# Kernel optimization log

Hardware: AMD Instinct MI355X
Metric: run time of the kernel (lower is better)

## Reference

```python
import jax, jax.numpy as jnp
import numpy as np

DIM = 1024


def setup_inputs() -> dict:
    key = jax.random.key(0)
    k1, k2, k3, k4 = jax.random.split(key, 4)
    B, T, S, D = 32, 512, 1024, DIM
    inp = {
        "input": jax.random.normal(k1, (B, T, D), dtype=jnp.float32),
        "context": jax.random.normal(k2, (B, S, D), dtype=jnp.float32),
        # linear_in: nn.Linear(dim, dim, bias=False) -> weight [D, D]
        "W_in": jax.random.normal(k3, (D, D), dtype=jnp.float32) / np.sqrt(D),
        # linear_out: nn.Linear(2*dim, dim, bias=False for 'general') -> weight [D, 2D]
        "W_out": jax.random.normal(k4, (D, 2 * D), dtype=jnp.float32) / np.sqrt(2 * D),
    }
    return inp


def reference(input, context, W_in, W_out):
    # score: general -> h_t = linear_in(input); align = bmm(h_t, context^T)
    h_t = jnp.einsum("btd,ed->bte", input, W_in)              # [B,T,D]
    align = jnp.einsum("btd,bsd->bts", h_t, context)          # [B,T,S]
    align_vectors = jax.nn.softmax(align, axis=-1)            # [B,T,S]
    c = jnp.einsum("bts,bsd->btd", align_vectors, context)    # [B,T,D]
    concat_c = jnp.concatenate([c, input], axis=2)            # [B,T,2D]
    attn_h = jnp.tanh(jnp.einsum("btf,df->btd", concat_c, W_out))  # [B,T,D]
    # multi-step path: transpose to (tgt_len, batch, ...)
    attn_h = jnp.transpose(attn_h, (1, 0, 2))
    concat_c = jnp.transpose(concat_c, (1, 0, 2))
    align_vectors = jnp.transpose(align_vectors, (1, 0, 2))
    return attn_h, align_vectors, concat_c
```

## Files before the change

### kernel.cpp

```cpp
#include <hip/hip_runtime.h>
#include <cmath>

#define BATCH 32
#define TLEN  512
#define SLEN  1024
#define DIM   1024

#define BM 128
#define BN 128
#define BK 32

typedef _Float16 h8 __attribute__((ext_vector_type(8)));
typedef _Float16 h4 __attribute__((ext_vector_type(4)));
typedef _Float16 h2 __attribute__((ext_vector_type(2)));
typedef float f4 __attribute__((ext_vector_type(4)));


__device__ __forceinline__ void gload16(const _Float16* g, _Float16* l) {
  __builtin_amdgcn_global_load_lds(
      (const __attribute__((address_space(1))) unsigned int*)g,
      (__attribute__((address_space(3))) unsigned int*)l, 16, 0, 0);
}

template <int EPI>
__global__ __launch_bounds__(256) void gemm16(
    const _Float16* __restrict__ A, const _Float16* __restrict__ Bm,
    float* __restrict__ C, _Float16* __restrict__ C16, int K,
    long lda, long ldb, long ldc, long ldc16,
    long strideA, long strideB, long strideC, long strideC16) {
  __shared__ _Float16 As[BM * BK];
  __shared__ _Float16 Bs[BN * BK];

  const int bz = blockIdx.z;
  A += (long)bz * strideA;
  Bm += (long)bz * strideB;

  const int m0 = blockIdx.y * BM;
  const int n0 = blockIdx.x * BN;
  const int tid = threadIdx.x;
  const int lane = tid & 63;
  const int wave = tid >> 6;
  const int q = lane >> 4;
  const int r = lane & 15;
  const int wm = (wave >> 1) * 64;
  const int wn = (wave & 1) * 64;

  f4 acc[4][4];
#pragma unroll
  for (int i = 0; i < 4; ++i)
#pragma unroll
    for (int j = 0; j < 4; ++j) acc[i][j] = (f4){0.f, 0.f, 0.f, 0.f};

  const int c0 = wave * 64 + lane;
  const int c1 = 256 + wave * 64 + lane;
  const _Float16* gA0 = A + (long)(m0 + (c0 >> 2)) * lda + (c0 & 3) * 8;
  const _Float16* gA1 = A + (long)(m0 + (c1 >> 2)) * lda + (c1 & 3) * 8;
  const _Float16* gB0 = Bm + (long)(n0 + (c0 >> 2)) * ldb + (c0 & 3) * 8;
  const _Float16* gB1 = Bm + (long)(n0 + (c1 >> 2)) * ldb + (c1 & 3) * 8;
  _Float16* lA0 = As + wave * 512;
  _Float16* lA1 = As + 2048 + wave * 512;
  _Float16* lB0 = Bs + wave * 512;
  _Float16* lB1 = Bs + 2048 + wave * 512;

  for (int k0 = 0; k0 < K; k0 += BK) {
    gload16(gA0 + k0, lA0);
    gload16(gA1 + k0, lA1);
    gload16(gB0 + k0, lB0);
    gload16(gB1 + k0, lB1);
    __syncthreads();

    h8 av[4], bv[4];
#pragma unroll
    for (int mt = 0; mt < 4; ++mt)
      av[mt] = *(const h8*)&As[(wm + mt * 16 + r) * BK + q * 8];
#pragma unroll
    for (int nt = 0; nt < 4; ++nt)
      bv[nt] = *(const h8*)&Bs[(wn + nt * 16 + r) * BK + q * 8];
#pragma unroll
    for (int mt = 0; mt < 4; ++mt)
#pragma unroll
      for (int nt = 0; nt < 4; ++nt)
        acc[mt][nt] = __builtin_amdgcn_mfma_f32_16x16x32_f16(
            av[mt], bv[nt], acc[mt][nt], 0, 0, 0);
    __syncthreads();
  }

#pragma unroll
  for (int mt = 0; mt < 4; ++mt) {
#pragma unroll
    for (int nt = 0; nt < 4; ++nt) {
#pragma unroll
      for (int i = 0; i < 4; ++i) {
        float x = acc[mt][nt][i];
        const long row = m0 + wm + mt * 16 + q * 4 + i;
        const long col = n0 + wn + nt * 16 + r;
        if constexpr (EPI == 1) x = tanhf(x);
        if constexpr (EPI == 0 || EPI == 1 || EPI == 3)
          C[(long)bz * strideC + row * ldc + col] = x;
        if constexpr (EPI == 2 || EPI == 3)
          C16[(long)bz * strideC16 + row * ldc16 + col] = (_Float16)x;
      }
    }
  }
}

__global__ __launch_bounds__(256) void cvt_f32_f16(
    const float* __restrict__ in, _Float16* __restrict__ out, long n) {
  long i = ((long)blockIdx.x * 256 + threadIdx.x) * 4;
  const long stride = (long)gridDim.x * 1024;
  for (; i < n; i += stride) {
    float4 v = *(const float4*)(in + i);
    h4 hv = {(_Float16)v.x, (_Float16)v.y, (_Float16)v.z, (_Float16)v.w};
    *(h4*)(out + i) = hv;
  }
}

#define CTPAD 66
__global__ __launch_bounds__(256) void ctx_cvt(
    const float* __restrict__ ctx, _Float16* __restrict__ c16,
    _Float16* __restrict__ c16t) {
  __shared__ _Float16 tile[64 * CTPAD];
  const int b = blockIdx.z;
  const int s0 = blockIdx.y * 64;
  const int d0 = blockIdx.x * 64;
  const int tr = threadIdx.x >> 4;
  const int tc = (threadIdx.x & 15) * 4;
#pragma unroll
  for (int i = 0; i < 4; ++i) {
    const int s = i * 16 + tr;
    float4 v = *(const float4*)(ctx + ((long)b * SLEN + s0 + s) * DIM + d0 + tc);
    h4 hv = {(_Float16)v.x, (_Float16)v.y, (_Float16)v.z, (_Float16)v.w};
    *(h4*)(c16 + ((long)b * SLEN + s0 + s) * DIM + d0 + tc) = hv;
    tile[s * CTPAD + tc] = hv.x;
    tile[s * CTPAD + tc + 1] = hv.y;
    tile[s * CTPAD + tc + 2] = hv.z;
    tile[s * CTPAD + tc + 3] = hv.w;
  }
  __syncthreads();
#pragma unroll
  for (int i = 0; i < 4; ++i) {
    const int d = i * 16 + tr;
    h4 hv = {tile[tc * CTPAD + d], tile[(tc + 1) * CTPAD + d],
             tile[(tc + 2) * CTPAD + d], tile[(tc + 3) * CTPAD + d]};
    *(h4*)(c16t + ((long)b * DIM + d0 + d) * SLEN + s0 + tc) = hv;
  }
}


#define AS_LD 40
#define B2_LD 134

template <bool B_IS_NT, bool TANH>
__global__ __launch_bounds__(256) void gemm_f16(
    const float* __restrict__ A, const float* __restrict__ Bm,
    float* __restrict__ C, int M, int N, int K, long lda, long ldb, long ldc,
    long strideA, long strideB, long strideC) {
  __shared__ _Float16 As[BM * AS_LD];
  __shared__ _Float16 Bs[BM * AS_LD];

  const int bz = blockIdx.z;
  A += (long)bz * strideA;
  Bm += (long)bz * strideB;
  C += (long)bz * strideC;

  const int m0 = blockIdx.y * BM;
  const int n0 = blockIdx.x * BN;
  const int tid = threadIdx.x;
  const int lane = tid & 63;
  const int wave = tid >> 6;
  const int wm = (wave >> 1) * 64;
  const int wn = (wave & 1) * 64;
  const int q = lane >> 4;
  const int r = lane & 15;

  f4 acc[4][4];
#pragma unroll
  for (int i = 0; i < 4; ++i)
#pragma unroll
    for (int j = 0; j < 4; ++j) acc[i][j] = (f4){0.f, 0.f, 0.f, 0.f};

  const int srow = tid >> 3;
  const int skq = (tid & 7) * 4;
  const int nrow = tid >> 5;
  const int nnq = (tid & 31) * 4;

  for (int k0 = 0; k0 < K; k0 += BK) {
#pragma unroll
    for (int it = 0; it < 4; ++it) {
      const int row = it * 32 + srow;
      f4 v = *(const f4*)(A + (long)(m0 + row) * lda + k0 + skq);
      h4 hv = {(_Float16)v.x, (_Float16)v.y, (_Float16)v.z, (_Float16)v.w};
      *(h4*)&As[row * AS_LD + skq] = hv;
    }
    if (B_IS_NT) {
#pragma unroll
      for (int it = 0; it < 4; ++it) {
        const int row = it * 32 + srow;
        f4 v = *(const f4*)(Bm + (long)(n0 + row) * ldb + k0 + skq);
        h4 hv = {(_Float16)v.x, (_Float16)v.y, (_Float16)v.z, (_Float16)v.w};
        *(h4*)&Bs[row * AS_LD + skq] = hv;
      }
    } else {
#pragma unroll
      for (int it = 0; it < 4; ++it) {
        const int krow = it * 8 + nrow;
        f4 v = *(const f4*)(Bm + (long)(k0 + krow) * ldb + n0 + nnq);
        _Float16* p = &Bs[krow * B2_LD + nnq];
        *(h2*)p = (h2){(_Float16)v.x, (_Float16)v.y};
        *(h2*)(p + 2) = (h2){(_Float16)v.z, (_Float16)v.w};
      }
    }
    __syncthreads();

    h8 av[4], bv[4];
#pragma unroll
    for (int mt = 0; mt < 4; ++mt)
      av[mt] = *(const h8*)&As[(wm + mt * 16 + r) * AS_LD + q * 8];
    if (B_IS_NT) {
#pragma unroll
      for (int nt = 0; nt < 4; ++nt)
        bv[nt] = *(const h8*)&Bs[(wn + nt * 16 + r) * AS_LD + q * 8];
    } else {
#pragma unroll
      for (int nt = 0; nt < 4; ++nt) {
        h8 t;
#pragma unroll
        for (int j = 0; j < 8; ++j)
          t[j] = Bs[(q * 8 + j) * B2_LD + wn + nt * 16 + r];
        bv[nt] = t;
      }
    }
#pragma unroll
    for (int mt = 0; mt < 4; ++mt)
#pragma unroll
      for (int nt = 0; nt < 4; ++nt)
        acc[mt][nt] = __builtin_amdgcn_mfma_f32_16x16x32_f16(
            av[mt], bv[nt], acc[mt][nt], 0, 0, 0);
    __syncthreads();
  }

#pragma unroll
  for (int mt = 0; mt < 4; ++mt) {
#pragma unroll
    for (int nt = 0; nt < 4; ++nt) {
#pragma unroll
      for (int i = 0; i < 4; ++i) {
        float x = acc[mt][nt][i];
        if (TANH) x = tanhf(x);
        C[(long)(m0 + wm + mt * 16 + q * 4 + i) * ldc + n0 + wn + nt * 16 + r] = x;
      }
    }
  }
}


__global__ __launch_bounds__(256) void softmax_kernel(
    float* __restrict__ data, _Float16* __restrict__ p16) {
  float* row = data + (long)blockIdx.x * SLEN;
  const int tid = threadIdx.x;
  float4 v = ((float4*)row)[tid];
  float m = fmaxf(fmaxf(v.x, v.y), fmaxf(v.z, v.w));
#pragma unroll
  for (int off = 32; off > 0; off >>= 1) m = fmaxf(m, __shfl_xor(m, off));
  __shared__ float redm[4];
  __shared__ float reds[4];
  if ((tid & 63) == 0) redm[tid >> 6] = m;
  __syncthreads();
  m = fmaxf(fmaxf(redm[0], redm[1]), fmaxf(redm[2], redm[3]));
  v.x = expf(v.x - m);
  v.y = expf(v.y - m);
  v.z = expf(v.z - m);
  v.w = expf(v.w - m);
  float s = v.x + v.y + v.z + v.w;
#pragma unroll
  for (int off = 32; off > 0; off >>= 1) s += __shfl_xor(s, off);
  if ((tid & 63) == 0) reds[tid >> 6] = s;
  __syncthreads();
  s = reds[0] + reds[1] + reds[2] + reds[3];
  const float inv = 1.0f / s;
  v.x *= inv;
  v.y *= inv;
  v.z *= inv;
  v.w *= inv;
  ((float4*)row)[tid] = v;
  if (p16) {
    h4 hv = {(_Float16)v.x, (_Float16)v.y, (_Float16)v.z, (_Float16)v.w};
    *(h4*)(p16 + (long)blockIdx.x * SLEN + tid * 4) = hv;
  }
}

__global__ __launch_bounds__(256) void concat_copy_kernel(
    const float* __restrict__ in, float* __restrict__ concat,
    _Float16* __restrict__ c16) {
  const int bt = blockIdx.x;
  const int b = bt >> 9;
  const int t = bt & 511;
  const float4 v = ((const float4*)(in + (long)bt * DIM))[threadIdx.x];
  const long off = ((long)t * BATCH + b) * (2 * DIM) + DIM;
  ((float4*)(concat + off))[threadIdx.x] = v;
  if (c16) {
    h4 hv = {(_Float16)v.x, (_Float16)v.y, (_Float16)v.z, (_Float16)v.w};
    *(h4*)(c16 + off + threadIdx.x * 4) = hv;
  }
}


extern "C" void kernel_launch(void* const* d_in, const int* in_sizes, int n_in,
                              void* d_out, int out_size, void* d_ws,
                              size_t ws_size, hipStream_t stream) {
  const float* input = (const float*)d_in[0];
  const float* context = (const float*)d_in[1];
  const float* W_in = (const float*)d_in[2];
  const float* W_out = (const float*)d_in[3];

  float* out = (float*)d_out;
  float* attn_h = out;
  float* align = out + (long)TLEN * BATCH * DIM;
  float* concat = align + (long)TLEN * BATCH * SLEN;

  const long BT = (long)BATCH * TLEN;
  const long ND = (long)BATCH * TLEN * DIM;

  const size_t WS_NEED = (size_t)3 * 67108864 + 4194304;

  if (d_ws != nullptr && ws_size >= WS_NEED) {
    _Float16* ctx16 = (_Float16*)d_ws;
    _Float16* ctx16t = ctx16 + (long)BATCH * SLEN * DIM;
    _Float16* cat16 = ctx16t + (long)BATCH * SLEN * DIM;
    _Float16* wout16 = cat16 + (long)TLEN * BATCH * 2 * DIM;
    _Float16* in16 = (_Float16*)align;
    _Float16* win16 = in16 + ND;
    _Float16* ht16 = (_Float16*)attn_h;
    _Float16* p16 = ht16 + ND;

    cvt_f32_f16<<<2048, 256, 0, stream>>>(input, in16, ND);
    cvt_f32_f16<<<1024, 256, 0, stream>>>(W_in, win16, (long)DIM * DIM);
    cvt_f32_f16<<<2048, 256, 0, stream>>>(W_out, wout16, (long)DIM * 2 * DIM);
    ctx_cvt<<<dim3(16, 16, BATCH), 256, 0, stream>>>(context, ctx16, ctx16t);

    gemm16<2><<<dim3(DIM / BN, BT / BM, 1), 256, 0, stream>>>(
        in16, win16, nullptr, ht16, DIM,
         DIM,  DIM,  0,  DIM, 0, 0, 0, 0);

    gemm16<0><<<dim3(SLEN / BN, TLEN / BM, BATCH), 256, 0, stream>>>(
        ht16, ctx16, align, nullptr, DIM,
         DIM,  DIM,  (long)BATCH * SLEN,  0,
         (long)TLEN * DIM,  (long)SLEN * DIM,  SLEN, 0);

    softmax_kernel<<<(int)BT, 256, 0, stream>>>(align, p16);

    gemm16<3><<<dim3(DIM / BN, TLEN / BM, BATCH), 256, 0, stream>>>(
        p16, ctx16t, concat, cat16, SLEN,
         (long)BATCH * SLEN,  SLEN,
         (long)BATCH * 2 * DIM,  (long)BATCH * 2 * DIM,
         SLEN,  (long)DIM * SLEN,  2 * DIM,  2 * DIM);

    concat_copy_kernel<<<(int)BT, 256, 0, stream>>>(input, concat, cat16);

    gemm16<1><<<dim3(DIM / BN, BT / BM, 1), 256, 0, stream>>>(
        cat16, wout16, attn_h, nullptr, 2 * DIM,
         2 * DIM,  2 * DIM,  DIM,  0, 0, 0, 0, 0);
    return;
  }

  float* h_t = attn_h;

  gemm_f16<true, false><<<dim3(DIM / BN, BT / BM, 1), 256, 0, stream>>>(
      input, W_in, h_t, (int)BT, DIM, DIM, DIM, DIM, DIM, 0, 0, 0);

  gemm_f16<true, false><<<dim3(SLEN / BN, TLEN / BM, BATCH), 256, 0, stream>>>(
      h_t, context, align, TLEN, SLEN, DIM, DIM, DIM, (long)BATCH * SLEN,
      (long)TLEN * DIM, (long)SLEN * DIM, SLEN);

  softmax_kernel<<<(int)BT, 256, 0, stream>>>(align, nullptr);

  gemm_f16<false, false><<<dim3(DIM / BN, TLEN / BM, BATCH), 256, 0, stream>>>(
      align, context, concat, TLEN, DIM, SLEN, (long)BATCH * SLEN, DIM,
      (long)BATCH * 2 * DIM, SLEN, (long)SLEN * DIM, 2 * DIM);

  concat_copy_kernel<<<(int)BT, 256, 0, stream>>>(input, concat, nullptr);

  gemm_f16<true, true><<<dim3(DIM / BN, BT / BM, 1), 256, 0, stream>>>(
      concat, W_out, attn_h, (int)BT, DIM, 2 * DIM, 2 * DIM, 2 * DIM, DIM,
      0, 0, 0);
}
```

Baseline: 826.0 us.

## Double GEMM K-tile with XOR-swizzled LDS, fuse converts and concat copy

The f16 GEMM K-step goes from 32 to 64, and LDS uses an XOR swizzle on the 16-byte chunks to avoid bank conflicts on the MFMA operand reads. The three f32-to-f16 conversion launches are merged into one kernel. The concat copy of the input is folded into the epilogue of the context GEMM, and the ctx transpose writes its LDS tile with vector stores. This cuts loop iterations, barriers and launch overhead, but doubles shared memory per block, which may lower occupancy.

```diff
diff --git a/kernel.cpp b/kernel.cpp
--- a/kernel.cpp
+++ b/kernel.cpp
@@ -8,7 +8,7 @@
 
 #define BM 128
 #define BN 128
-#define BK 32
+#define BK2 64
 
 typedef _Float16 h8 __attribute__((ext_vector_type(8)));
 typedef _Float16 h4 __attribute__((ext_vector_type(4)));
@@ -27,9 +27,10 @@
     const _Float16* __restrict__ A, const _Float16* __restrict__ Bm,
     float* __restrict__ C, _Float16* __restrict__ C16, int K,
     long lda, long ldb, long ldc, long ldc16,
-    long strideA, long strideB, long strideC, long strideC16) {
-  __shared__ _Float16 As[BM * BK];
-  __shared__ _Float16 Bs[BN * BK];
+    long strideA, long strideB, long strideC, long strideC16,
+    const float* __restrict__ Xin) {
+  __shared__ _Float16 As[BM * BK2];
+  __shared__ _Float16 Bs[BM * BK2];
 
   const int bz = blockIdx.z;
   A += (long)bz * strideA;
@@ -51,37 +52,50 @@
 #pragma unroll
     for (int j = 0; j < 4; ++j) acc[i][j] = (f4){0.f, 0.f, 0.f, 0.f};
 
-  const int c0 = wave * 64 + lane;
-  const int c1 = 256 + wave * 64 + lane;
-  const _Float16* gA0 = A + (long)(m0 + (c0 >> 2)) * lda + (c0 & 3) * 8;
-  const _Float16* gA1 = A + (long)(m0 + (c1 >> 2)) * lda + (c1 & 3) * 8;
-  const _Float16* gB0 = Bm + (long)(n0 + (c0 >> 2)) * ldb + (c0 & 3) * 8;
-  const _Float16* gB1 = Bm + (long)(n0 + (c1 >> 2)) * ldb + (c1 & 3) * 8;
-  _Float16* lA0 = As + wave * 512;
-  _Float16* lA1 = As + 2048 + wave * 512;
-  _Float16* lB0 = Bs + wave * 512;
-  _Float16* lB1 = Bs + 2048 + wave * 512;
-
-  for (int k0 = 0; k0 < K; k0 += BK) {
-    gload16(gA0 + k0, lA0);
-    gload16(gA1 + k0, lA1);
-    gload16(gB0 + k0, lB0);
-    gload16(gB1 + k0, lB1);
+  const _Float16* gA[4];
+  const _Float16* gB[4];
+  _Float16* lA[4];
+  _Float16* lB[4];
+#pragma unroll
+  for (int i = 0; i < 4; ++i) {
+    const int c = i * 256 + tid;
+    const int row = c >> 3;
+    const int j = (c & 7) ^ (row & 7);
+    gA[i] = A + (long)(m0 + row) * lda + j * 8;
+    gB[i] = Bm + (long)(n0 + row) * ldb + j * 8;
+    lA[i] = As + i * 2048 + wave * 512;
+    lB[i] = Bs + i * 2048 + wave * 512;
+  }
+
+  for (int k0 = 0; k0 < K; k0 += BK2) {
+#pragma unroll
+    for (int i = 0; i < 4; ++i) gload16(gA[i] + k0, lA[i]);
+#pragma unroll
+    for (int i = 0; i < 4; ++i) gload16(gB[i] + k0, lB[i]);
     __syncthreads();
 
-    h8 av[4], bv[4];
-#pragma unroll
-    for (int mt = 0; mt < 4; ++mt)
-      av[mt] = *(const h8*)&As[(wm + mt * 16 + r) * BK + q * 8];
-#pragma unroll
-    for (int nt = 0; nt < 4; ++nt)
-      bv[nt] = *(const h8*)&Bs[(wn + nt * 16 + r) * BK + q * 8];
-#pragma unroll
-    for (int mt = 0; mt < 4; ++mt)
-#pragma unroll
-      for (int nt = 0; nt < 4; ++nt)
-        acc[mt][nt] = __builtin_amdgcn_mfma_f32_16x16x32_f16(
-            av[mt], bv[nt], acc[mt][nt], 0, 0, 0);
+#pragma unroll
+    for (int kk = 0; kk < 2; ++kk) {
+      h8 av[4], bv[4];
+#pragma unroll
+      for (int mt = 0; mt < 4; ++mt) {
+        const int row = wm + mt * 16 + r;
+        const int u = (kk * 4 + q) ^ (r & 7);
+        av[mt] = *(const h8*)&As[row * BK2 + u * 8];
+      }
+#pragma unroll
+      for (int nt = 0; nt < 4; ++nt) {
+        const int row = wn + nt * 16 + r;
+        const int u = (kk * 4 + q) ^ (r & 7);
+        bv[nt] = *(const h8*)&Bs[row * BK2 + u * 8];
+      }
+#pragma unroll
+      for (int mt = 0; mt < 4; ++mt)
+#pragma unroll
+        for (int nt = 0; nt < 4; ++nt)
+          acc[mt][nt] = __builtin_amdgcn_mfma_f32_16x16x32_f16(
+              av[mt], bv[nt], acc[mt][nt], 0, 0, 0);
+    }
     __syncthreads();
   }
 
@@ -95,27 +109,54 @@
         const long row = m0 + wm + mt * 16 + q * 4 + i;
         const long col = n0 + wn + nt * 16 + r;
         if constexpr (EPI == 1) x = tanhf(x);
-        if constexpr (EPI == 0 || EPI == 1 || EPI == 3)
+        if constexpr (EPI != 2)
           C[(long)bz * strideC + row * ldc + col] = x;
-        if constexpr (EPI == 2 || EPI == 3)
+        if constexpr (EPI >= 2)
           C16[(long)bz * strideC16 + row * ldc16 + col] = (_Float16)x;
       }
     }
   }
-}
-
-__global__ __launch_bounds__(256) void cvt_f32_f16(
-    const float* __restrict__ in, _Float16* __restrict__ out, long n) {
-  long i = ((long)blockIdx.x * 256 + threadIdx.x) * 4;
-  const long stride = (long)gridDim.x * 1024;
+
+  if constexpr (EPI == 4) {
+#pragma unroll
+    for (int it = 0; it < 16; ++it) {
+      const int idx = it * 256 + tid;
+      const int row = idx >> 5;
+      const int c4 = (idx & 31) * 4;
+      const f4 v = *(const f4*)(Xin + ((long)bz * TLEN + m0 + row) * DIM +
+                                n0 + c4);
+      const long off = (long)bz * strideC + (long)(m0 + row) * ldc + DIM +
+                       n0 + c4;
+      *(f4*)(C + off) = v;
+      h4 hv = {(_Float16)v.x, (_Float16)v.y, (_Float16)v.z, (_Float16)v.w};
+      *(h4*)(C16 + (long)bz * strideC16 + (long)(m0 + row) * ldc16 + DIM +
+             n0 + c4) = hv;
+    }
+  }
+}
+
+__global__ __launch_bounds__(256) void cvt3(
+    const float* __restrict__ in, _Float16* __restrict__ out,
+    const float* __restrict__ in2, _Float16* __restrict__ out2,
+    const float* __restrict__ in3, _Float16* __restrict__ out3) {
+  const int b = blockIdx.x;
+  const float* src;
+  _Float16* dst;
+  long n;
+  int b0, nb;
+  if (b < 384) { src = in;  dst = out;  n = 16777216; b0 = 0;   nb = 384; }
+  else if (b < 408) { src = in2; dst = out2; n = 1048576; b0 = 384; nb = 24; }
+  else { src = in3; dst = out3; n = 2097152; b0 = 408; nb = 48; }
+  long i = ((long)(b - b0) * 256 + threadIdx.x) * 4;
+  const long stride = (long)nb * 1024;
   for (; i < n; i += stride) {
-    float4 v = *(const float4*)(in + i);
+    f4 v = *(const f4*)(src + i);
     h4 hv = {(_Float16)v.x, (_Float16)v.y, (_Float16)v.z, (_Float16)v.w};
-    *(h4*)(out + i) = hv;
-  }
-}
-
-#define CTPAD 66
+    *(h4*)(dst + i) = hv;
+  }
+}
+
+#define CTPAD 68
 __global__ __launch_bounds__(256) void ctx_cvt(
     const float* __restrict__ ctx, _Float16* __restrict__ c16,
     _Float16* __restrict__ c16t) {
@@ -131,10 +172,7 @@
     float4 v = *(const float4*)(ctx + ((long)b * SLEN + s0 + s) * DIM + d0 + tc);
     h4 hv = {(_Float16)v.x, (_Float16)v.y, (_Float16)v.z, (_Float16)v.w};
     *(h4*)(c16 + ((long)b * SLEN + s0 + s) * DIM + d0 + tc) = hv;
-    tile[s * CTPAD + tc] = hv.x;
-    tile[s * CTPAD + tc + 1] = hv.y;
-    tile[s * CTPAD + tc + 2] = hv.z;
-    tile[s * CTPAD + tc + 3] = hv.w;
+    *(h4*)&tile[s * CTPAD + tc] = hv;
   }
   __syncthreads();
 #pragma unroll
@@ -149,6 +187,7 @@
 
 #define AS_LD 40
 #define B2_LD 134
+#define BKF 32
 
 template <bool B_IS_NT, bool TANH>
 __global__ __launch_bounds__(256) void gemm_f16(
@@ -184,7 +223,7 @@
   const int nrow = tid >> 5;
   const int nnq = (tid & 31) * 4;
 
-  for (int k0 = 0; k0 < K; k0 += BK) {
+  for (int k0 = 0; k0 < K; k0 += BKF) {
 #pragma unroll
     for (int it = 0; it < 4; ++it) {
       const int row = it * 32 + srow;
@@ -333,33 +372,33 @@
     _Float16* ht16 = (_Float16*)attn_h;
     _Float16* p16 = ht16 + ND;
 
-    cvt_f32_f16<<<2048, 256, 0, stream>>>(input, in16, ND);
-    cvt_f32_f16<<<1024, 256, 0, stream>>>(W_in, win16, (long)DIM * DIM);
-    cvt_f32_f16<<<2048, 256, 0, stream>>>(W_out, wout16, (long)DIM * 2 * DIM);
+    cvt3<<<456, 256, 0, stream>>>(input, in16, W_in, win16, W_out, wout16);
     ctx_cvt<<<dim3(16, 16, BATCH), 256, 0, stream>>>(context, ctx16, ctx16t);
 
     gemm16<2><<<dim3(DIM / BN, BT / BM, 1), 256, 0, stream>>>(
         in16, win16, nullptr, ht16, DIM,
-         DIM,  DIM,  0,  DIM, 0, 0, 0, 0);
+         DIM,  DIM,  0,  DIM, 0, 0, 0, 0,
+        nullptr);
 
     gemm16<0><<<dim3(SLEN / BN, TLEN / BM, BATCH), 256, 0, stream>>>(
         ht16, ctx16, align, nullptr, DIM,
          DIM,  DIM,  (long)BATCH * SLEN,  0,
-         (long)TLEN * DIM,  (long)SLEN * DIM,  SLEN, 0);
+         (long)TLEN * DIM,  (long)SLEN * DIM,  SLEN, 0,
+        nullptr);
 
     softmax_kernel<<<(int)BT, 256, 0, stream>>>(align, p16);
 
-    gemm16<3><<<dim3(DIM / BN, TLEN / BM, BATCH), 256, 0, stream>>>(
+    gemm16<4><<<dim3(DIM / BN, TLEN / BM, BATCH), 256, 0, stream>>>(
         p16, ctx16t, concat, cat16, SLEN,
          (long)BATCH * SLEN,  SLEN,
          (long)BATCH * 2 * DIM,  (long)BATCH * 2 * DIM,
-         SLEN,  (long)DIM * SLEN,  2 * DIM,  2 * DIM);
-
-    concat_copy_kernel<<<(int)BT, 256, 0, stream>>>(input, concat, cat16);
+         SLEN,  (long)DIM * SLEN,  2 * DIM,
+         2 * DIM, input);
 
     gemm16<1><<<dim3(DIM / BN, BT / BM, 1), 256, 0, stream>>>(
         cat16, wout16, attn_h, nullptr, 2 * DIM,
-         2 * DIM,  2 * DIM,  DIM,  0, 0, 0, 0, 0);
+         2 * DIM,  2 * DIM,  DIM,  0, 0, 0, 0, 0,
+        nullptr);
     return;
   }
 
```

New measurement: 765.4 us. 1.08x faster.
